# Kernel optimization log

Hardware: AMD Instinct MI355X
Metric: run time of the kernel (lower is better)

## Reference

```python
import jax, jax.numpy as jnp
import numpy as np

B, N, K = 8, 4096, 64          # graphs, nodes per graph, clusters
E_PER = 65536                   # edges per graph (avg degree 16)
EPS = 1e-15


def gcn_conv(x, W, b, src, dst, num_nodes):
    """PyG GCNConv: add self-loops, symmetric deg^-1/2 normalization, sum-aggregate at dst."""
    h = x @ W
    loop = jnp.arange(num_nodes, dtype=src.dtype)
    s_all = jnp.concatenate([src, loop])
    d_all = jnp.concatenate([dst, loop])
    deg = jax.ops.segment_sum(jnp.ones(d_all.shape[0], dtype=h.dtype), d_all, num_segments=num_nodes)
    dis = jnp.where(deg > 0, jax.lax.rsqrt(deg), 0.0)
    msg = h[s_all] * (dis[s_all] * dis[d_all])[:, None]
    return jax.ops.segment_sum(msg, d_all, num_segments=num_nodes) + b


def setup_inputs() -> dict:
    key = jax.random.key(0)
    ks = jax.random.split(key, 12)
    F_in, H, F_out = 128, 128, 128
    x = jax.random.normal(ks[0], (B * N, F_in), dtype=jnp.float32)
    # within-graph random edges, then offset to global node ids
    local = jax.random.randint(ks[1], (2, B * E_PER), 0, N, dtype=jnp.int32)
    offs = jnp.repeat(jnp.arange(B, dtype=jnp.int32) * N, E_PER)
    edge_index = local + offs[None, :]
    batch = jnp.repeat(jnp.arange(B, dtype=jnp.int32), N)

    def lin(k, i, o):
        return (jax.random.normal(k, (i, o), dtype=jnp.float32) / np.float32(np.sqrt(i)))

    return {
        "x": x, "edge_index": edge_index, "batch": batch,
        "W1": lin(ks[2], F_in, H), "b1": jnp.zeros((H,), jnp.float32),
        "W2": lin(ks[3], H, H),    "b2": jnp.zeros((H,), jnp.float32),
        "Wa1": lin(ks[4], H, H),   "ba1": jnp.zeros((H,), jnp.float32),
        "Wa2": lin(ks[5], H, K),   "ba2": jnp.zeros((K,), jnp.float32),
        "Wo": lin(ks[6], H, F_out), "bo": jnp.zeros((F_out,), jnp.float32),
    }


def reference(x, edge_index, batch, W1, b1, W2, b2, Wa1, ba1, Wa2, ba2, Wo, bo):
    num_nodes = B * N
    src, dst = edge_index[0], edge_index[1]
    # two GCN layers (dropout inactive in eval mode)
    h = jax.nn.relu(gcn_conv(x, W1, b1, src, dst, num_nodes))
    h = gcn_conv(h, W2, b2, src, dst, num_nodes)
    # assignment MLP + softmax (module applies softmax; dense_mincut_pool re-applies it)
    s = jax.nn.softmax(jnp.tanh(h @ Wa1 + ba1) @ Wa2 + ba2, axis=-1)
    # to_dense_adj: scatter edges into [B, N, N]
    g = src // N
    adj = jnp.zeros((B, N, N), h.dtype).at[g, src % N, dst % N].add(1.0)
    # to_dense_batch: equal-size graphs -> reshape (mask all True)
    x_d = h.reshape(B, N, -1)
    s_d = jax.nn.softmax(s.reshape(B, N, K), axis=-1)  # PyG internal softmax (double softmax, faithful)
    # dense_mincut_pool
    out = jnp.einsum('bnk,bnf->bkf', s_d, x_d)              # s^T x : [B,K,F]
    As = jnp.einsum('bnm,bmk->bnk', adj, s_d)
    out_adj = jnp.einsum('bnk,bnj->bkj', s_d, As)           # s^T A s : [B,K,K]
    mincut_num = jnp.trace(out_adj, axis1=-2, axis2=-1)
    d_flat = adj.sum(-1)                                    # node degrees
    mincut_den = jnp.einsum('bnk,bn,bnk->b', s_d, d_flat, s_d)  # trace(s^T D s)
    mincut_loss = jnp.mean(-(mincut_num / mincut_den))
    ss = jnp.einsum('bnk,bnj->bkj', s_d, s_d)
    ss_n = jnp.linalg.norm(ss, axis=(-1, -2), keepdims=True)
    i_s = jnp.eye(K, dtype=ss.dtype)
    ortho_loss = jnp.mean(jnp.linalg.norm(ss / ss_n - i_s / jnp.sqrt(jnp.float32(K)), axis=(-1, -2)))
    # zero diagonal + symmetric degree normalization of pooled adj
    out_adj = out_adj * (1.0 - i_s)
    d = jnp.sqrt(out_adj.sum(-1))[:, None, :] + EPS         # [B,1,K]
    out_adj = out_adj / d / jnp.swapaxes(d, 1, 2)
    # output projection
    pooled_x = jax.nn.relu(out.reshape(-1, out.shape[-1]) @ Wo + bo)  # [B*K, F_out]
    pooled_batch = jnp.repeat(jnp.arange(B), K)
    # pooled_adj returned densely: pooled_edge_index == nonzero(pooled_adj > 0) (dynamic shape)
    return pooled_x, out_adj, pooled_batch, mincut_loss, ortho_loss
```

## Files before the change

### kernel.cpp

```cpp
#include <hip/hip_runtime.h>

#define NNODES 32768
#define NEDGES 524288
#define KCL 64
#define CPG 16

typedef _Float16 half8v __attribute__((ext_vector_type(8)));
typedef _Float16 half4v __attribute__((ext_vector_type(4)));
typedef float floatx4 __attribute__((ext_vector_type(4)));

#define WT1_OFF   0
#define WT2_OFF   16384
#define WTA1_OFF  32768
#define WTA2_OFF  49152
#define WTO_OFF   57344
#define WT_TOTAL  73728

__device__ __forceinline__ float wave_sum(float v) {
#pragma unroll
  for (int off = 32; off > 0; off >>= 1) v += __shfl_xor(v, off, 64);
  return v;
}

__global__ __launch_bounds__(256) void hist2_kernel(const int* __restrict__ src, const int* __restrict__ dst,
                                                    int* __restrict__ pIn,
                                                    const float* __restrict__ W1, const float* __restrict__ W2,
                                                    const float* __restrict__ Wa1, const float* __restrict__ Wa2,
                                                    const float* __restrict__ Wo, _Float16* __restrict__ wt16) {
  __shared__ int hIn[4096];
  const int t = threadIdx.x;
  const int g = blockIdx.x & 7;
  const int chunk = blockIdx.x >> 3;
  const int ebase = (g << 16) + (chunk << 12);
  const int nbase = g << 12;
  for (int i = t; i < 4096; i += 256) hIn[i] = 0;
  __syncthreads();
  {
    int tg = blockIdx.x * 256 + t;
#pragma unroll
    for (int i = 0; i < 3; i++) {
      int id = tg + i * 32768;
      if (id < WT_TOTAL) {
        const float* W; int base, BN;
        if (id < 16384)      { W = W1;  base = WT1_OFF;  BN = 128; }
        else if (id < 32768) { W = W2;  base = WT2_OFF;  BN = 128; }
        else if (id < 49152) { W = Wa1; base = WTA1_OFF; BN = 128; }
        else if (id < 57344) { W = Wa2; base = WTA2_OFF; BN = 64; }
        else                 { W = Wo;  base = WTO_OFF;  BN = 128; }
        int m = id - base;
        int k = m / BN, n = m % BN;
        wt16[base + n * 128 + k] = (_Float16)W[m];
      }
    }
  }
  const int4* dst4 = reinterpret_cast<const int4*>(dst + ebase);
#pragma unroll
  for (int i = 0; i < 4; ++i) {
    int4 d = dst4[i * 256 + t];
    atomicAdd(&hIn[d.x - nbase], 1);
    atomicAdd(&hIn[d.y - nbase], 1);
    atomicAdd(&hIn[d.z - nbase], 1);
    atomicAdd(&hIn[d.w - nbase], 1);
  }
  __syncthreads();
  int* dIn = pIn + ((size_t)(g * CPG + chunk) << 12);
  for (int i = t; i < 4096; i += 256) dIn[i] = hIn[i];
}

__global__ __launch_bounds__(1024) void scan2_kernel(const int* __restrict__ pIn, int* __restrict__ offs,
                                                     int* __restrict__ cbase, float* __restrict__ dis) {
  __shared__ int part[1024];
  const int t = threadIdx.x;
  const int g = blockIdx.x;
  int tot[4];
  int s = 0;
#pragma unroll
  for (int j = 0; j < 4; ++j) {
    int l = t * 4 + j;
    int cnt = 0;
#pragma unroll
    for (int c = 0; c < CPG; ++c) cnt += pIn[(((size_t)(g * CPG + c)) << 12) + l];
    tot[j] = cnt;
    s += cnt;
  }
  part[t] = s;
  __syncthreads();
  for (int off = 1; off < 1024; off <<= 1) {
    int add = (t >= off) ? part[t - off] : 0;
    __syncthreads();
    part[t] += add;
    __syncthreads();
  }
  int run = (g << 16) + ((t == 0) ? 0 : part[t - 1]);
#pragma unroll
  for (int j = 0; j < 4; ++j) {
    int l = t * 4 + j;
    int n = (g << 12) + l;
    offs[n] = run;
    dis[n] = rsqrtf((float)tot[j] + 1.0f);
    int running = run;
#pragma unroll
    for (int c = 0; c < CPG; ++c) {
      size_t idx = (((size_t)(g * CPG + c)) << 12) + l;
      cbase[idx] = running;
      running += pIn[idx];
    }
    run += tot[j];
  }
  if (g == 0 && t == 0) offs[NNODES] = NEDGES;
}

__global__ __launch_bounds__(256) void scatter2_kernel(const int* __restrict__ src, const int* __restrict__ dst,
                                                       const int* __restrict__ cbase, int* __restrict__ ssrc) {
  __shared__ int cur[4096];
  const int t = threadIdx.x;
  const int g = blockIdx.x & 7;
  const int chunk = blockIdx.x >> 3;
  const int ebase = (g << 16) + (chunk << 12);
  const int nbase = g << 12;
  const int* cb = cbase + ((size_t)(g * CPG + chunk) << 12);
  for (int i = t; i < 4096; i += 256) cur[i] = cb[i];
  __syncthreads();
  const int4* dst4 = reinterpret_cast<const int4*>(dst + ebase);
  const int4* src4 = reinterpret_cast<const int4*>(src + ebase);
#pragma unroll
  for (int i = 0; i < 4; ++i) {
    int4 d = dst4[i * 256 + t];
    int4 s = src4[i * 256 + t];
    int p0 = atomicAdd(&cur[d.x - nbase], 1); ssrc[p0] = s.x;
    int p1 = atomicAdd(&cur[d.y - nbase], 1); ssrc[p1] = s.y;
    int p2 = atomicAdd(&cur[d.z - nbase], 1); ssrc[p2] = s.z;
    int p3 = atomicAdd(&cur[d.w - nbase], 1); ssrc[p3] = s.w;
  }
}

template <int ACT, int BIAS, int SCALE, int AFP32>
__global__ __launch_bounds__(256) void mgemm_kernel(const void* __restrict__ Ain, const _Float16* __restrict__ WT16,
                                                    const float* __restrict__ bias, const float* __restrict__ rowscale,
                                                    _Float16* __restrict__ Cout) {
  __shared__ _Float16 WT[128][136];
  const int t = threadIdx.x;
#pragma unroll
  for (int i = 0; i < 8; i++) {
    int idx = i * 256 + t;
    int n = idx >> 4, k8 = (idx & 15) << 3;
    *reinterpret_cast<half8v*>(&WT[n][k8]) = *reinterpret_cast<const half8v*>(&WT16[n * 128 + k8]);
  }
  __syncthreads();
  const int lane = t & 63;
  const int quad = lane >> 4, l16 = lane & 15;
  const long rowbase = (long)(blockIdx.x & 7) * 4096 + (long)(blockIdx.x >> 3) * 128 + (t >> 6) * 32;
  half8v af[2][4];
#pragma unroll
  for (int rt = 0; rt < 2; rt++)
#pragma unroll
    for (int kt = 0; kt < 4; kt++) {
      if (AFP32) {
        const float* A32 = (const float*)Ain;
        const float* p = A32 + (rowbase + rt * 16 + l16) * 128 + kt * 32 + quad * 8;
        float4 p0 = *reinterpret_cast<const float4*>(p);
        float4 p1 = *reinterpret_cast<const float4*>(p + 4);
        half8v h = {(_Float16)p0.x, (_Float16)p0.y, (_Float16)p0.z, (_Float16)p0.w,
                    (_Float16)p1.x, (_Float16)p1.y, (_Float16)p1.z, (_Float16)p1.w};
        af[rt][kt] = h;
      } else {
        const _Float16* A16 = (const _Float16*)Ain;
        af[rt][kt] = *reinterpret_cast<const half8v*>(A16 + (rowbase + rt * 16 + l16) * 128 + kt * 32 + quad * 8);
      }
    }
  floatx4 acc[2][8];
#pragma unroll
  for (int rt = 0; rt < 2; rt++)
#pragma unroll
    for (int ct = 0; ct < 8; ct++) acc[rt][ct] = {0.f, 0.f, 0.f, 0.f};
#pragma unroll
  for (int kt = 0; kt < 4; kt++) {
    half8v bf[8];
#pragma unroll
    for (int ct = 0; ct < 8; ct++)
      bf[ct] = *reinterpret_cast<const half8v*>(&WT[ct * 16 + l16][kt * 32 + quad * 8]);
#pragma unroll
    for (int rt = 0; rt < 2; rt++)
#pragma unroll
      for (int ct = 0; ct < 8; ct++)
        acc[rt][ct] = __builtin_amdgcn_mfma_f32_16x16x32_f16(af[rt][kt], bf[ct], acc[rt][ct], 0, 0, 0);
  }
#pragma unroll
  for (int rt = 0; rt < 2; rt++) {
#pragma unroll
    for (int r = 0; r < 4; r++) {
      long row = rowbase + rt * 16 + quad * 4 + r;
      float sc = SCALE ? rowscale[row] : 1.f;
#pragma unroll
      for (int ct = 0; ct < 8; ct++) {
        float v = acc[rt][ct][r];
        if (SCALE) v *= sc;
        if (BIAS) v += bias[ct * 16 + l16];
        if (ACT == 1) v = fmaxf(v, 0.f);
        Cout[row * 128 + ct * 16 + l16] = (_Float16)v;
      }
    }
  }
}

__global__ __launch_bounds__(256) void mlp_kernel(const _Float16* __restrict__ h2, const _Float16* __restrict__ wta1,
                                                  const _Float16* __restrict__ wta2, const float* __restrict__ ba1,
                                                  const float* __restrict__ ba2, _Float16* __restrict__ sh) {
  __shared__ _Float16 WT1[128][136];
  __shared__ _Float16 WT2[64][136];
  __shared__ _Float16 Z[128][136];
  const int t = threadIdx.x;
#pragma unroll
  for (int i = 0; i < 8; i++) {
    int idx = i * 256 + t;
    int n = idx >> 4, k8 = (idx & 15) << 3;
    *reinterpret_cast<half8v*>(&WT1[n][k8]) = *reinterpret_cast<const half8v*>(&wta1[n * 128 + k8]);
  }
#pragma unroll
  for (int i = 0; i < 4; i++) {
    int idx = i * 256 + t;
    int n = idx >> 4, k8 = (idx & 15) << 3;
    *reinterpret_cast<half8v*>(&WT2[n][k8]) = *reinterpret_cast<const half8v*>(&wta2[n * 128 + k8]);
  }
  __syncthreads();
  const int lane = t & 63;
  const int quad = lane >> 4, l16 = lane & 15;
  const int w = t >> 6;
  const long rowbase = (long)(blockIdx.x & 7) * 4096 + (long)(blockIdx.x >> 3) * 128 + w * 32;
  half8v af[2][4];
#pragma unroll
  for (int rt = 0; rt < 2; rt++)
#pragma unroll
    for (int kt = 0; kt < 4; kt++)
      af[rt][kt] = *reinterpret_cast<const half8v*>(h2 + (rowbase + rt * 16 + l16) * 128 + kt * 32 + quad * 8);
  {
    floatx4 acc[2][8];
#pragma unroll
    for (int rt = 0; rt < 2; rt++)
#pragma unroll
      for (int ct = 0; ct < 8; ct++) acc[rt][ct] = {0.f, 0.f, 0.f, 0.f};
#pragma unroll
    for (int kt = 0; kt < 4; kt++) {
      half8v bf[8];
#pragma unroll
      for (int ct = 0; ct < 8; ct++)
        bf[ct] = *reinterpret_cast<const half8v*>(&WT1[ct * 16 + l16][kt * 32 + quad * 8]);
#pragma unroll
      for (int rt = 0; rt < 2; rt++)
#pragma unroll
        for (int ct = 0; ct < 8; ct++)
          acc[rt][ct] = __builtin_amdgcn_mfma_f32_16x16x32_f16(af[rt][kt], bf[ct], acc[rt][ct], 0, 0, 0);
    }
#pragma unroll
    for (int rt = 0; rt < 2; rt++)
#pragma unroll
      for (int r = 0; r < 4; r++) {
        int lrow = w * 32 + rt * 16 + quad * 4 + r;
#pragma unroll
        for (int ct = 0; ct < 8; ct++) {
          float v = tanhf(acc[rt][ct][r] + ba1[ct * 16 + l16]);
          Z[lrow][ct * 16 + l16] = (_Float16)v;
        }
      }
  }
  __syncthreads();
  half8v af2[2][4];
#pragma unroll
  for (int rt = 0; rt < 2; rt++)
#pragma unroll
    for (int kt = 0; kt < 4; kt++)
      af2[rt][kt] = *reinterpret_cast<const half8v*>(&Z[w * 32 + rt * 16 + l16][kt * 32 + quad * 8]);
  floatx4 acc2[2][4];
#pragma unroll
  for (int rt = 0; rt < 2; rt++)
#pragma unroll
    for (int ct = 0; ct < 4; ct++) acc2[rt][ct] = {0.f, 0.f, 0.f, 0.f};
#pragma unroll
  for (int kt = 0; kt < 4; kt++) {
    half8v bf[4];
#pragma unroll
    for (int ct = 0; ct < 4; ct++)
      bf[ct] = *reinterpret_cast<const half8v*>(&WT2[ct * 16 + l16][kt * 32 + quad * 8]);
#pragma unroll
    for (int rt = 0; rt < 2; rt++)
#pragma unroll
      for (int ct = 0; ct < 4; ct++)
        acc2[rt][ct] = __builtin_amdgcn_mfma_f32_16x16x32_f16(af2[rt][kt], bf[ct], acc2[rt][ct], 0, 0, 0);
  }
#pragma unroll
  for (int rt = 0; rt < 2; rt++) {
#pragma unroll
    for (int r = 0; r < 4; r++) {
      long row = rowbase + rt * 16 + quad * 4 + r;
      float v[4];
#pragma unroll
      for (int ct = 0; ct < 4; ct++) v[ct] = acc2[rt][ct][r] + ba2[ct * 16 + l16];
      float m = fmaxf(fmaxf(v[0], v[1]), fmaxf(v[2], v[3]));
#pragma unroll
      for (int off = 1; off <= 8; off <<= 1) m = fmaxf(m, __shfl_xor(m, off, 64));
      float se = 0.f;
#pragma unroll
      for (int ct = 0; ct < 4; ct++) { v[ct] = __expf(v[ct] - m); se += v[ct]; }
#pragma unroll
      for (int off = 1; off <= 8; off <<= 1) se += __shfl_xor(se, off, 64);
      float inv = 1.0f / se;
#pragma unroll
      for (int ct = 0; ct < 4; ct++) v[ct] *= inv;
      float m2 = fmaxf(fmaxf(v[0], v[1]), fmaxf(v[2], v[3]));
#pragma unroll
      for (int off = 1; off <= 8; off <<= 1) m2 = fmaxf(m2, __shfl_xor(m2, off, 64));
      float se2 = 0.f;
#pragma unroll
      for (int ct = 0; ct < 4; ct++) { v[ct] = __expf(v[ct] - m2); se2 += v[ct]; }
#pragma unroll
      for (int off = 1; off <= 8; off <<= 1) se2 += __shfl_xor(se2, off, 64);
      float inv2 = 1.0f / se2;
#pragma unroll
      for (int ct = 0; ct < 4; ct++) sh[row * 64 + ct * 16 + l16] = (_Float16)(v[ct] * inv2);
    }
  }
}

__global__ __launch_bounds__(256) void aggregate_kernel(const _Float16* __restrict__ hs, const float* __restrict__ dis,
                                                        const int* __restrict__ offs, const int* __restrict__ ssrc,
                                                        const float* __restrict__ bias, _Float16* __restrict__ outh,
                                                        int relu) {
  const int lane = threadIdx.x & 63;
  const int b = blockIdx.x;
  const int node = ((b & 7) << 12) + ((b >> 3) << 2) + (threadIdx.x >> 6);
  const int q = lane >> 4;
  const int fl = (lane & 15) * 8;
  const int e0 = offs[node], e1 = offs[node + 1];
  float fa[8];
#pragma unroll
  for (int j = 0; j < 8; j++) fa[j] = 0.f;
  int e = e0;
  for (; e + 32 <= e1; e += 32) {
    int s[8];
#pragma unroll
    for (int jj = 0; jj < 8; jj++) s[jj] = ssrc[e + jj * 4 + q];
#pragma unroll
    for (int jj = 0; jj < 8; jj++) {
      half8v v = *reinterpret_cast<const half8v*>(hs + (size_t)s[jj] * 128 + fl);
#pragma unroll
      for (int j = 0; j < 8; j++) fa[j] += (float)v[j];
    }
  }
  if (e < e1) {
    int last = e1 - 1;
    int s[8]; bool m[8];
#pragma unroll
    for (int jj = 0; jj < 8; jj++) {
      int idx = e + jj * 4 + q;
      m[jj] = idx < e1;
      s[jj] = ssrc[idx < last ? idx : last];
    }
#pragma unroll
    for (int jj = 0; jj < 8; jj++) {
      half8v v = *reinterpret_cast<const half8v*>(hs + (size_t)s[jj] * 128 + fl);
      if (m[jj]) {
#pragma unroll
        for (int j = 0; j < 8; j++) fa[j] += (float)v[j];
      }
    }
  }
#pragma unroll
  for (int j = 0; j < 8; j++) {
    fa[j] += __shfl_xor(fa[j], 16, 64);
    fa[j] += __shfl_xor(fa[j], 32, 64);
  }
  if (q == 0) {
    float dn = dis[node];
    half8v self = *reinterpret_cast<const half8v*>(hs + (size_t)node * 128 + fl);
    float4 b0 = *reinterpret_cast<const float4*>(bias + fl);
    float4 b1 = *reinterpret_cast<const float4*>(bias + fl + 4);
    float bb[8] = {b0.x, b0.y, b0.z, b0.w, b1.x, b1.y, b1.z, b1.w};
    half8v r;
#pragma unroll
    for (int j = 0; j < 8; j++) {
      float v = fmaf(fa[j] + (float)self[j], dn, bb[j]);
      if (relu) v = fmaxf(v, 0.f);
      r[j] = (_Float16)v;
    }
    *reinterpret_cast<half8v*>(outh + (size_t)node * 128 + fl) = r;
  }
}

__global__ __launch_bounds__(512) void fused_atb_kernel(const _Float16* __restrict__ sh, const _Float16* __restrict__ h2,
                                                        const int* __restrict__ offs, const int* __restrict__ ssrc,
                                                        float* __restrict__ dnp, float* __restrict__ pF) {
  __shared__ float Xs[32][64];
  __shared__ float Ys[32][256];
  __shared__ _Float16 Gs[128][64];
  const int t = threadIdx.x;
  const int g = blockIdx.x & 7, chunk = blockIdx.x >> 3;
  const int n0 = g * 4096 + chunk * 128;
  const int w = t >> 6;
  const int lane = t & 63;

  {
    const int q = lane >> 3;
    const int fl = (lane & 7) * 8;
    for (int i = 0; i < 16; ++i) {
      const int node = n0 + w * 16 + i;
      const int e0 = offs[node], e1 = offs[node + 1];
      float fa[8];
      float sq = 0.f;
#pragma unroll
      for (int j = 0; j < 8; j++) fa[j] = 0.f;
      int e = e0;
      for (; e + 32 <= e1; e += 32) {
        int s[4];
#pragma unroll
        for (int jj = 0; jj < 4; jj++) s[jj] = ssrc[e + jj * 8 + q];
#pragma unroll
        for (int jj = 0; jj < 4; jj++) {
          half8v v = *reinterpret_cast<const half8v*>(sh + (size_t)s[jj] * 64 + fl);
#pragma unroll
          for (int j = 0; j < 8; j++) {
            float f = (float)v[j];
            fa[j] += f;
            sq = fmaf(f, f, sq);
          }
        }
      }
      if (e < e1) {
        int last = e1 - 1;
        int s[4]; bool m[4];
#pragma unroll
        for (int jj = 0; jj < 4; jj++) {
          int idx = e + jj * 8 + q;
          m[jj] = idx < e1;
          s[jj] = ssrc[idx < last ? idx : last];
        }
#pragma unroll
        for (int jj = 0; jj < 4; jj++) {
          half8v v = *reinterpret_cast<const half8v*>(sh + (size_t)s[jj] * 64 + fl);
          if (m[jj]) {
#pragma unroll
            for (int j = 0; j < 8; j++) {
              float f = (float)v[j];
              fa[j] += f;
              sq = fmaf(f, f, sq);
            }
          }
        }
      }
#pragma unroll
      for (int j = 0; j < 8; j++) {
        fa[j] += __shfl_xor(fa[j], 8, 64);
        fa[j] += __shfl_xor(fa[j], 16, 64);
        fa[j] += __shfl_xor(fa[j], 32, 64);
      }
      float den = wave_sum(sq);
      if (lane == 0) dnp[node] = den;
      if (q == 0) {
        half8v r;
#pragma unroll
        for (int j = 0; j < 8; j++) r[j] = (_Float16)fa[j];
        *reinterpret_cast<half8v*>(&Gs[w * 16 + i][fl]) = r;
      }
    }
  }
  __syncthreads();

  const int rg = w;
  const int cl = lane;
  float acc[8][4];
#pragma unroll
  for (int r = 0; r < 8; r++)
#pragma unroll
    for (int j = 0; j < 4; j++) acc[r][j] = 0.f;

  for (int kt = 0; kt < 4; ++kt) {
    const int nb = n0 + kt * 32;
    {
      int k = t >> 4, c = (t & 15) * 4;
      half4v hv = *reinterpret_cast<const half4v*>(&sh[(size_t)(nb + k) * 64 + c]);
      float4 val = {(float)hv[0], (float)hv[1], (float)hv[2], (float)hv[3]};
      *reinterpret_cast<float4*>(&Xs[k][c]) = val;
    }
#pragma unroll
    for (int it = 0; it < 4; ++it) {
      int slot = it * 512 + t;
      int k = slot >> 6, c = (slot & 63) * 4;
      half4v hv;
      if (c < 64)       hv = *reinterpret_cast<const half4v*>(&Gs[kt * 32 + k][c]);
      else if (c < 128) hv = *reinterpret_cast<const half4v*>(&sh[(size_t)(nb + k) * 64 + (c - 64)]);
      else              hv = *reinterpret_cast<const half4v*>(&h2[(size_t)(nb + k) * 128 + (c - 128)]);
      float4 val = {(float)hv[0], (float)hv[1], (float)hv[2], (float)hv[3]};
      *reinterpret_cast<float4*>(&Ys[k][c]) = val;
    }
    __syncthreads();
#pragma unroll
    for (int k = 0; k < 32; ++k) {
      float4 b4 = *reinterpret_cast<const float4*>(&Ys[k][cl * 4]);
      float4 a0 = *reinterpret_cast<const float4*>(&Xs[k][rg * 8]);
      float4 a1 = *reinterpret_cast<const float4*>(&Xs[k][rg * 8 + 4]);
      float a[8] = {a0.x, a0.y, a0.z, a0.w, a1.x, a1.y, a1.z, a1.w};
#pragma unroll
      for (int r = 0; r < 8; r++) {
        acc[r][0] = fmaf(a[r], b4.x, acc[r][0]);
        acc[r][1] = fmaf(a[r], b4.y, acc[r][1]);
        acc[r][2] = fmaf(a[r], b4.z, acc[r][2]);
        acc[r][3] = fmaf(a[r], b4.w, acc[r][3]);
      }
    }
    __syncthreads();
  }
  float* dst = pF + (size_t)blockIdx.x * 16384;
#pragma unroll
  for (int r = 0; r < 8; r++) {
    float4 o4 = {acc[r][0], acc[r][1], acc[r][2], acc[r][3]};
    *reinterpret_cast<float4*>(&dst[(rg * 8 + r) * 256 + cl * 4]) = o4;
  }
}

__global__ __launch_bounds__(256) void merge_kernel(const float* __restrict__ pF, float* __restrict__ oadj,
                                                    float* __restrict__ ssb, _Float16* __restrict__ outp16) {
  int g = blockIdx.x & 7;
  int o4 = (blockIdx.x >> 3) * 256 + threadIdx.x;
  float sx = 0.f, sy = 0.f, sz = 0.f, sw = 0.f;
#pragma unroll
  for (int q = 0; q < 32; ++q) {
    float4 v = *reinterpret_cast<const float4*>(pF + (size_t)(q * 8 + g) * 16384 + o4 * 4);
    sx += v.x; sy += v.y; sz += v.z; sw += v.w;
  }
  int row = o4 >> 6;
  int c = (o4 & 63) * 4;
  if (c < 64) {
    float4 o = {sx, sy, sz, sw};
    *reinterpret_cast<float4*>(&oadj[g * 4096 + row * 64 + c]) = o;
  } else if (c < 128) {
    float4 o = {sx, sy, sz, sw};
    *reinterpret_cast<float4*>(&ssb[g * 4096 + row * 64 + (c - 64)]) = o;
  } else {
    half4v h = {(_Float16)sx, (_Float16)sy, (_Float16)sz, (_Float16)sw};
    *reinterpret_cast<half4v*>(&outp16[g * 8192 + row * 128 + (c - 128)]) = h;
  }
}

__global__ __launch_bounds__(256) void epilogue2_kernel(const float* __restrict__ oadj, const float* __restrict__ ssb,
                                                        const _Float16* __restrict__ outp16, const _Float16* __restrict__ wto,
                                                        const float* __restrict__ bo, const float* __restrict__ dn,
                                                        float* __restrict__ out) {
  __shared__ _Float16 outpS[64][136];
  __shared__ _Float16 WoT[128][136];
  __shared__ float red[256];
  __shared__ float rowsum[64];
  __shared__ float dw[4], w1[4], w2[4], w3[4];
  const int g = blockIdx.x, t = threadIdx.x;

#pragma unroll
  for (int i = 0; i < 8; i++) {
    int idx = i * 256 + t;
    int n = idx >> 4, k8 = (idx & 15) << 3;
    *reinterpret_cast<half8v*>(&WoT[n][k8]) = *reinterpret_cast<const half8v*>(&wto[n * 128 + k8]);
  }
#pragma unroll
  for (int i = 0; i < 4; i++) {
    int idx = i * 256 + t;
    int orow = idx >> 4, c8 = (idx & 15) * 8;
    half8v v = *reinterpret_cast<const half8v*>(&outp16[g * 8192 + orow * 128 + c8]);
    *reinterpret_cast<half8v*>(&outpS[orow][c8]) = v;
  }

  const int row = t >> 2, p = t & 3;
  float Areg[16];
  float trs_p = 0.f, ssq_p = 0.f;
#pragma unroll
  for (int c4 = 0; c4 < 4; c4++) {
    float4 a = *reinterpret_cast<const float4*>(&oadj[g * 4096 + row * 64 + p * 16 + c4 * 4]);
    Areg[c4 * 4 + 0] = a.x; Areg[c4 * 4 + 1] = a.y; Areg[c4 * 4 + 2] = a.z; Areg[c4 * 4 + 3] = a.w;
    float4 s = *reinterpret_cast<const float4*>(&ssb[g * 4096 + row * 64 + p * 16 + c4 * 4]);
    float vv[4] = {s.x, s.y, s.z, s.w};
#pragma unroll
    for (int jj = 0; jj < 4; jj++) {
      ssq_p += vv[jj] * vv[jj];
      int col = p * 16 + c4 * 4 + jj;
      if (col == row) trs_p += vv[jj];
    }
  }
  float da = 0.f;
#pragma unroll
  for (int i = 0; i < 16; i++) da += dn[g * 4096 + i * 256 + t];
  float dws = wave_sum(da);
  if ((t & 63) == 0) dw[t >> 6] = dws;

  float rs = 0.f, tra = 0.f;
#pragma unroll
  for (int c = 0; c < 16; c++) {
    int j = p * 16 + c;
    if (j == row) tra += Areg[c];
    else rs += Areg[c];
  }
  red[t] = rs;
  __syncthreads();
  if (p == 0) rowsum[row] = red[t] + red[t + 1] + red[t + 2] + red[t + 3];
  float v1 = wave_sum(tra), v2 = wave_sum(trs_p), v3 = wave_sum(ssq_p);
  if ((t & 63) == 0) { int w = t >> 6; w1[w] = v1; w2[w] = v2; w3[w] = v3; }
  __syncthreads();
  if (t == 0) {
    float TRA = w1[0] + w1[1] + w1[2] + w1[3];
    float TRS = w2[0] + w2[1] + w2[2] + w2[3];
    float SSQ = w3[0] + w3[1] + w3[2] + w3[3];
    float DEN = dw[0] + dw[1] + dw[2] + dw[3];
    atomicAdd(&out[98816], -(TRA / DEN) * 0.125f);
    float ssn = sqrtf(SSQ);
    atomicAdd(&out[98817], sqrtf(2.0f - TRS / (4.0f * ssn)) * 0.125f);
  }
  float di = sqrtf(rowsum[row]) + 1e-15f;
#pragma unroll
  for (int c = 0; c < 16; c++) {
    int j = p * 16 + c;
    float v = (j == row) ? 0.f : Areg[c];
    float dj = sqrtf(rowsum[j]) + 1e-15f;
    out[65536 + g * 4096 + row * 64 + j] = v / (di * dj);
  }
  if (t < 64) out[98304 + g * 64 + t] = (float)g;

  const int lane = t & 63;
  const int quad = lane >> 4, l16 = lane & 15;
  const int w = t >> 6;
  floatx4 acc[8];
#pragma unroll
  for (int ct = 0; ct < 8; ct++) acc[ct] = {0.f, 0.f, 0.f, 0.f};
#pragma unroll
  for (int kt = 0; kt < 4; kt++) {
    half8v af = *reinterpret_cast<const half8v*>(&outpS[w * 16 + l16][kt * 32 + quad * 8]);
#pragma unroll
    for (int ct = 0; ct < 8; ct++) {
      half8v bf = *reinterpret_cast<const half8v*>(&WoT[ct * 16 + l16][kt * 32 + quad * 8]);
      acc[ct] = __builtin_amdgcn_mfma_f32_16x16x32_f16(af, bf, acc[ct], 0, 0, 0);
    }
  }
#pragma unroll
  for (int r = 0; r < 4; r++) {
    int orow = w * 16 + quad * 4 + r;
#pragma unroll
    for (int ct = 0; ct < 8; ct++) {
      int col = ct * 16 + l16;
      float v = fmaxf(acc[ct][r] + bo[col], 0.f);
      out[(g * 64 + orow) * 128 + col] = v;
    }
  }
}

extern "C" void kernel_launch(void* const* d_in, const int* in_sizes, int n_in,
                              void* d_out, int out_size, void* d_ws, size_t ws_size,
                              hipStream_t stream) {
  const float* x   = (const float*)d_in[0];
  const int*   ei  = (const int*)d_in[1];
  const float* W1  = (const float*)d_in[3];
  const float* b1  = (const float*)d_in[4];
  const float* W2  = (const float*)d_in[5];
  const float* b2  = (const float*)d_in[6];
  const float* Wa1 = (const float*)d_in[7];
  const float* ba1 = (const float*)d_in[8];
  const float* Wa2 = (const float*)d_in[9];
  const float* ba2 = (const float*)d_in[10];
  const float* Wo  = (const float*)d_in[11];
  const float* bo  = (const float*)d_in[12];
  const int* src = ei;
  const int* dst = ei + NEDGES;
  float* out = (float*)d_out;

  char* ws = (char*)d_ws;
  size_t o = 0;
  auto alloc = [&](size_t bytes) -> void* {
    void* p = ws + o;
    o += (bytes + 255) & ~(size_t)255;
    return p;
  };
  _Float16* h16A = (_Float16*)alloc((size_t)NNODES * 128 * 2);
  _Float16* h16B = (_Float16*)alloc((size_t)NNODES * 128 * 2);
  _Float16* h16C = (_Float16*)alloc((size_t)NNODES * 128 * 2);
  _Float16* sh   = (_Float16*)alloc((size_t)NNODES * 64 * 2);
  float* pF    = (float*)alloc((size_t)256 * 16384 * 4);
  float* dis   = (float*)alloc((size_t)NNODES * 4);
  int* offs    = (int*)alloc((size_t)(NNODES + 1) * 4);
  int* ssrc    = (int*)alloc((size_t)NEDGES * 4);
  int* pIn     = (int*)alloc((size_t)8 * CPG * 4096 * 4);
  int* cbase   = (int*)alloc((size_t)8 * CPG * 4096 * 4);
  float* dn    = (float*)alloc((size_t)NNODES * 4);
  float* oadj  = (float*)alloc(8 * 4096 * 4);
  float* ssb   = (float*)alloc(8 * 4096 * 4);
  _Float16* outp16 = (_Float16*)alloc(8 * 8192 * 2);
  _Float16* wt16   = (_Float16*)alloc((size_t)WT_TOTAL * 2);

  hipMemsetAsync(out + 98816, 0, 2 * sizeof(float), stream);

  hist2_kernel<<<8 * CPG, 256, 0, stream>>>(src, dst, pIn, W1, W2, Wa1, Wa2, Wo, wt16);
  scan2_kernel<<<8, 1024, 0, stream>>>(pIn, offs, cbase, dis);
  scatter2_kernel<<<8 * CPG, 256, 0, stream>>>(src, dst, cbase, ssrc);

  mgemm_kernel<0, 0, 1, 1><<<NNODES / 128, 256, 0, stream>>>(x, wt16 + WT1_OFF, nullptr, dis, h16A);
  aggregate_kernel<<<NNODES / 4, 256, 0, stream>>>(h16A, dis, offs, ssrc, b1, h16B, 1);
  mgemm_kernel<0, 0, 1, 0><<<NNODES / 128, 256, 0, stream>>>(h16B, wt16 + WT2_OFF, nullptr, dis, h16A);
  aggregate_kernel<<<NNODES / 4, 256, 0, stream>>>(h16A, dis, offs, ssrc, b2, h16C, 0);

  mlp_kernel<<<NNODES / 128, 256, 0, stream>>>(h16C, wt16 + WTA1_OFF, wt16 + WTA2_OFF, ba1, ba2, sh);

  fused_atb_kernel<<<256, 512, 0, stream>>>(sh, h16C, offs, ssrc, dn, pF);
  merge_kernel<<<128, 256, 0, stream>>>(pF, oadj, ssb, outp16);
  epilogue2_kernel<<<8, 256, 0, stream>>>(oadj, ssb, outp16, wt16 + WTO_OFF, bo, dn, out);
}
```

Baseline: 227.1 us.

## Split gather out of fused ATB kernel and overlap weight staging with A loads

Moves the per-node neighbor gather of cluster assignments out of the 256-block fused kernel into its own kernel with one wave per node across 8192 blocks, writing an fp16 intermediate that the ATB GEMM kernel then reads. This is meant to fix the low parallelism of the gather phase, which previously ran over only 256 blocks with 16 serial nodes per wave. In exchange it adds a launch and a global round-trip for the gathered buffer. In the mgemm and mlp kernels, the LDS weight staging is moved after the A-fragment global loads so the two overlap, and the mlp kernel reuses one LDS buffer for both weight matrices, adding a barrier but lowering shared-memory use.

```diff
diff --git a/kernel.cpp b/kernel.cpp
--- a/kernel.cpp
+++ b/kernel.cpp
@@ -140,13 +140,6 @@
                                                     _Float16* __restrict__ Cout) {
   __shared__ _Float16 WT[128][136];
   const int t = threadIdx.x;
-#pragma unroll
-  for (int i = 0; i < 8; i++) {
-    int idx = i * 256 + t;
-    int n = idx >> 4, k8 = (idx & 15) << 3;
-    *reinterpret_cast<half8v*>(&WT[n][k8]) = *reinterpret_cast<const half8v*>(&WT16[n * 128 + k8]);
-  }
-  __syncthreads();
   const int lane = t & 63;
   const int quad = lane >> 4, l16 = lane & 15;
   const long rowbase = (long)(blockIdx.x & 7) * 4096 + (long)(blockIdx.x >> 3) * 128 + (t >> 6) * 32;
@@ -168,6 +161,13 @@
         af[rt][kt] = *reinterpret_cast<const half8v*>(A16 + (rowbase + rt * 16 + l16) * 128 + kt * 32 + quad * 8);
       }
     }
+#pragma unroll
+  for (int i = 0; i < 8; i++) {
+    int idx = i * 256 + t;
+    int n = idx >> 4, k8 = (idx & 15) << 3;
+    *reinterpret_cast<half8v*>(&WT[n][k8]) = *reinterpret_cast<const half8v*>(&WT16[n * 128 + k8]);
+  }
+  __syncthreads();
   floatx4 acc[2][8];
 #pragma unroll
   for (int rt = 0; rt < 2; rt++)
@@ -207,22 +207,8 @@
                                                   const _Float16* __restrict__ wta2, const float* __restrict__ ba1,
                                                   const float* __restrict__ ba2, _Float16* __restrict__ sh) {
   __shared__ _Float16 WT1[128][136];
-  __shared__ _Float16 WT2[64][136];
   __shared__ _Float16 Z[128][136];
   const int t = threadIdx.x;
-#pragma unroll
-  for (int i = 0; i < 8; i++) {
-    int idx = i * 256 + t;
-    int n = idx >> 4, k8 = (idx & 15) << 3;
-    *reinterpret_cast<half8v*>(&WT1[n][k8]) = *reinterpret_cast<const half8v*>(&wta1[n * 128 + k8]);
-  }
-#pragma unroll
-  for (int i = 0; i < 4; i++) {
-    int idx = i * 256 + t;
-    int n = idx >> 4, k8 = (idx & 15) << 3;
-    *reinterpret_cast<half8v*>(&WT2[n][k8]) = *reinterpret_cast<const half8v*>(&wta2[n * 128 + k8]);
-  }
-  __syncthreads();
   const int lane = t & 63;
   const int quad = lane >> 4, l16 = lane & 15;
   const int w = t >> 6;
@@ -233,6 +219,13 @@
 #pragma unroll
     for (int kt = 0; kt < 4; kt++)
       af[rt][kt] = *reinterpret_cast<const half8v*>(h2 + (rowbase + rt * 16 + l16) * 128 + kt * 32 + quad * 8);
+#pragma unroll
+  for (int i = 0; i < 8; i++) {
+    int idx = i * 256 + t;
+    int n = idx >> 4, k8 = (idx & 15) << 3;
+    *reinterpret_cast<half8v*>(&WT1[n][k8]) = *reinterpret_cast<const half8v*>(&wta1[n * 128 + k8]);
+  }
+  __syncthreads();
   {
     floatx4 acc[2][8];
 #pragma unroll
@@ -264,12 +257,19 @@
       }
   }
   __syncthreads();
+#pragma unroll
+  for (int i = 0; i < 4; i++) {
+    int idx = i * 256 + t;
+    int n = idx >> 4, k8 = (idx & 15) << 3;
+    *reinterpret_cast<half8v*>(&WT1[n][k8]) = *reinterpret_cast<const half8v*>(&wta2[n * 128 + k8]);
+  }
   half8v af2[2][4];
 #pragma unroll
   for (int rt = 0; rt < 2; rt++)
 #pragma unroll
     for (int kt = 0; kt < 4; kt++)
       af2[rt][kt] = *reinterpret_cast<const half8v*>(&Z[w * 32 + rt * 16 + l16][kt * 32 + quad * 8]);
+  __syncthreads();
   floatx4 acc2[2][4];
 #pragma unroll
   for (int rt = 0; rt < 2; rt++)
@@ -280,7 +280,7 @@
     half8v bf[4];
 #pragma unroll
     for (int ct = 0; ct < 4; ct++)
-      bf[ct] = *reinterpret_cast<const half8v*>(&WT2[ct * 16 + l16][kt * 32 + quad * 8]);
+      bf[ct] = *reinterpret_cast<const half8v*>(&WT1[ct * 16 + l16][kt * 32 + quad * 8]);
 #pragma unroll
     for (int rt = 0; rt < 2; rt++)
 #pragma unroll
@@ -386,86 +386,82 @@
   }
 }
 
-__global__ __launch_bounds__(512) void fused_atb_kernel(const _Float16* __restrict__ sh, const _Float16* __restrict__ h2,
-                                                        const int* __restrict__ offs, const int* __restrict__ ssrc,
-                                                        float* __restrict__ dnp, float* __restrict__ pF) {
+__global__ __launch_bounds__(256) void gather_kernel(const _Float16* __restrict__ sh, const int* __restrict__ offs,
+                                                     const int* __restrict__ ssrc, _Float16* __restrict__ Gh,
+                                                     float* __restrict__ dnp) {
+  const int lane = threadIdx.x & 63;
+  const int b = blockIdx.x;
+  const int node = ((b & 7) << 12) + ((b >> 3) << 2) + (threadIdx.x >> 6);
+  const int q = lane >> 3;
+  const int fl = (lane & 7) * 8;
+  const int e0 = offs[node], e1 = offs[node + 1];
+  float fa[8];
+  float sq = 0.f;
+#pragma unroll
+  for (int j = 0; j < 8; j++) fa[j] = 0.f;
+  int e = e0;
+  for (; e + 32 <= e1; e += 32) {
+    int s[4];
+#pragma unroll
+    for (int jj = 0; jj < 4; jj++) s[jj] = ssrc[e + jj * 8 + q];
+#pragma unroll
+    for (int jj = 0; jj < 4; jj++) {
+      half8v v = *reinterpret_cast<const half8v*>(sh + (size_t)s[jj] * 64 + fl);
+#pragma unroll
+      for (int j = 0; j < 8; j++) {
+        float f = (float)v[j];
+        fa[j] += f;
+        sq = fmaf(f, f, sq);
+      }
+    }
+  }
+  if (e < e1) {
+    int last = e1 - 1;
+    int s[4]; bool m[4];
+#pragma unroll
+    for (int jj = 0; jj < 4; jj++) {
+      int idx = e + jj * 8 + q;
+      m[jj] = idx < e1;
+      s[jj] = ssrc[idx < last ? idx : last];
+    }
+#pragma unroll
+    for (int jj = 0; jj < 4; jj++) {
+      half8v v = *reinterpret_cast<const half8v*>(sh + (size_t)s[jj] * 64 + fl);
+      if (m[jj]) {
+#pragma unroll
+        for (int j = 0; j < 8; j++) {
+          float f = (float)v[j];
+          fa[j] += f;
+          sq = fmaf(f, f, sq);
+        }
+      }
+    }
+  }
+#pragma unroll
+  for (int j = 0; j < 8; j++) {
+    fa[j] += __shfl_xor(fa[j], 8, 64);
+    fa[j] += __shfl_xor(fa[j], 16, 64);
+    fa[j] += __shfl_xor(fa[j], 32, 64);
+  }
+  float den = wave_sum(sq);
+  if (lane == 0) dnp[node] = den;
+  if (q == 0) {
+    half8v r;
+#pragma unroll
+    for (int j = 0; j < 8; j++) r[j] = (_Float16)fa[j];
+    *reinterpret_cast<half8v*>(Gh + (size_t)node * 64 + fl) = r;
+  }
+}
+
+__global__ __launch_bounds__(512) void atb_kernel(const _Float16* __restrict__ sh, const _Float16* __restrict__ Gh,
+                                                  const _Float16* __restrict__ h2, float* __restrict__ pF) {
   __shared__ float Xs[32][64];
   __shared__ float Ys[32][256];
-  __shared__ _Float16 Gs[128][64];
   const int t = threadIdx.x;
   const int g = blockIdx.x & 7, chunk = blockIdx.x >> 3;
   const int n0 = g * 4096 + chunk * 128;
-  const int w = t >> 6;
-  const int lane = t & 63;
-
-  {
-    const int q = lane >> 3;
-    const int fl = (lane & 7) * 8;
-    for (int i = 0; i < 16; ++i) {
-      const int node = n0 + w * 16 + i;
-      const int e0 = offs[node], e1 = offs[node + 1];
-      float fa[8];
-      float sq = 0.f;
-#pragma unroll
-      for (int j = 0; j < 8; j++) fa[j] = 0.f;
-      int e = e0;
-      for (; e + 32 <= e1; e += 32) {
-        int s[4];
-#pragma unroll
-        for (int jj = 0; jj < 4; jj++) s[jj] = ssrc[e + jj * 8 + q];
-#pragma unroll
-        for (int jj = 0; jj < 4; jj++) {
-          half8v v = *reinterpret_cast<const half8v*>(sh + (size_t)s[jj] * 64 + fl);
-#pragma unroll
-          for (int j = 0; j < 8; j++) {
-            float f = (float)v[j];
-            fa[j] += f;
-            sq = fmaf(f, f, sq);
-          }
-        }
-      }
-      if (e < e1) {
-        int last = e1 - 1;
-        int s[4]; bool m[4];
-#pragma unroll
-        for (int jj = 0; jj < 4; jj++) {
-          int idx = e + jj * 8 + q;
-          m[jj] = idx < e1;
-          s[jj] = ssrc[idx < last ? idx : last];
-        }
-#pragma unroll
-        for (int jj = 0; jj < 4; jj++) {
-          half8v v = *reinterpret_cast<const half8v*>(sh + (size_t)s[jj] * 64 + fl);
-          if (m[jj]) {
-#pragma unroll
-            for (int j = 0; j < 8; j++) {
-              float f = (float)v[j];
-              fa[j] += f;
-              sq = fmaf(f, f, sq);
-            }
-          }
-        }
-      }
-#pragma unroll
-      for (int j = 0; j < 8; j++) {
-        fa[j] += __shfl_xor(fa[j], 8, 64);
-        fa[j] += __shfl_xor(fa[j], 16, 64);
-        fa[j] += __shfl_xor(fa[j], 32, 64);
-      }
-      float den = wave_sum(sq);
-      if (lane == 0) dnp[node] = den;
-      if (q == 0) {
-        half8v r;
-#pragma unroll
-        for (int j = 0; j < 8; j++) r[j] = (_Float16)fa[j];
-        *reinterpret_cast<half8v*>(&Gs[w * 16 + i][fl]) = r;
-      }
-    }
-  }
-  __syncthreads();
-
-  const int rg = w;
-  const int cl = lane;
+  const int rg = t >> 6;
+  const int cl = t & 63;
   float acc[8][4];
 #pragma unroll
   for (int r = 0; r < 8; r++)
@@ -485,7 +481,7 @@
       int slot = it * 512 + t;
       int k = slot >> 6, c = (slot & 63) * 4;
       half4v hv;
-      if (c < 64)       hv = *reinterpret_cast<const half4v*>(&Gs[kt * 32 + k][c]);
+      if (c < 64)       hv = *reinterpret_cast<const half4v*>(&Gh[(size_t)(nb + k) * 64 + c]);
       else if (c < 128) hv = *reinterpret_cast<const half4v*>(&sh[(size_t)(nb + k) * 64 + (c - 64)]);
       else              hv = *reinterpret_cast<const half4v*>(&h2[(size_t)(nb + k) * 128 + (c - 128)]);
       float4 val = {(float)hv[0], (float)hv[1], (float)hv[2], (float)hv[3]};
@@ -676,6 +672,7 @@
   _Float16* h16B = (_Float16*)alloc((size_t)NNODES * 128 * 2);
   _Float16* h16C = (_Float16*)alloc((size_t)NNODES * 128 * 2);
   _Float16* sh   = (_Float16*)alloc((size_t)NNODES * 64 * 2);
+  _Float16* Gh   = (_Float16*)alloc((size_t)NNODES * 64 * 2);
   float* pF    = (float*)alloc((size_t)256 * 16384 * 4);
   float* dis   = (float*)alloc((size_t)NNODES * 4);
   int* offs    = (int*)alloc((size_t)(NNODES + 1) * 4);
@@ -701,7 +698,8 @@
 
   mlp_kernel<<<NNODES / 128, 256, 0, stream>>>(h16C, wt16 + WTA1_OFF, wt16 + WTA2_OFF, ba1, ba2, sh);
 
-  fused_atb_kernel<<<256, 512, 0, stream>>>(sh, h16C, offs, ssrc, dn, pF);
+  gather_kernel<<<NNODES / 4, 256, 0, stream>>>(sh, offs, ssrc, Gh, dn);
+  atb_kernel<<<256, 512, 0, stream>>>(sh, Gh, h16C, pF);
   merge_kernel<<<128, 256, 0, stream>>>(pF, oadj, ssb, outp16);
   epilogue2_kernel<<<8, 256, 0, stream>>>(oadj, ssb, outp16, wt16 + WTO_OFF, bo, dn, out);
 }
```

Result: no change. 222.6 us (-2.0%).
